# Kernel optimization log

Measured on AMD Instinct MI355X. Metric: run time of the kernel, lower is better.

## Reference

```python
import math
import jax, jax.numpy as jnp
import numpy as np

NEG_INF = -1e9


def maximum_path(neg_cent, text_len, spec_len):
    """Monotonic alignment search (VITS). neg_cent: [B, Ty(spec), Tx(text)].
    Returns hard path [B, Ty, Tx] (float32, 0/1)."""
    B, Ty, Tx = neg_cent.shape
    xs = jnp.arange(Tx)

    # Forward DP over spec frames y; carry = best cumulative value per text pos x.
    def fwd_step(value, inp):
        y, score = inp  # score: [B, Tx]
        diag = jnp.pad(value[:, :-1], ((0, 0), (1, 0)), constant_values=NEG_INF)
        d = diag > value  # move-diagonally indicator for backtracking
        new = score + jnp.maximum(value, diag)
        new = jnp.where(y == 0, jnp.where(xs == 0, score, NEG_INF), new)
        return new, d

    init = jnp.full((B, Tx), NEG_INF, dtype=neg_cent.dtype)
    _, dirs = jax.lax.scan(fwd_step, init,
                           (jnp.arange(Ty), jnp.swapaxes(neg_cent, 0, 1)))
    # dirs: [Ty, B, Tx] bool; dirs[y] compares row y-1 values (as in cython MAS).

    # Backtrack from (spec_len-1, text_len-1) down to y=0.
    def bwd_step(index, inp):
        y, d_row = inp  # index: [B] int32, d_row: [B, Tx]
        active = y < spec_len  # [B]
        row = jnp.where(active[:, None],
                        jax.nn.one_hot(index, Tx, dtype=jnp.float32), 0.0)
        d_at = jnp.take_along_axis(d_row, index[:, None], axis=1)[:, 0]
        move = (index != 0) & ((index == y) | d_at)
        index = jnp.where(active & move, index - 1, index)
        return index, row

    init_idx = text_len - 1
    _, path = jax.lax.scan(bwd_step, init_idx, (jnp.arange(Ty), dirs),
                           reverse=True)
    return jnp.swapaxes(path, 0, 1)  # [B, Ty, Tx]


def setup_inputs() -> dict:
    key = jax.random.key(0)
    ks = jax.random.split(key, 6)
    B, C, Tx, Ty = 8, 192, 512, 2048
    z_p = jax.random.normal(ks[0], (B, C, Ty), dtype=jnp.float32)
    m_p = jax.random.normal(ks[1], (B, C, Tx), dtype=jnp.float32)
    logs_p = 0.1 * jax.random.normal(ks[2], (B, C, Tx), dtype=jnp.float32)
    logs_q = 0.1 * jax.random.normal(ks[3], (B, C, Ty), dtype=jnp.float32)
    text_len = jax.random.randint(ks[4], (B,), Tx * 3 // 4, Tx + 1)
    spec_len = jax.random.randint(ks[5], (B,), Ty * 3 // 4, Ty + 1)
    text_mask = (jnp.arange(Tx)[None, :] < text_len[:, None]).astype(jnp.float32)[:, None, :]
    spec_mask = (jnp.arange(Ty)[None, :] < spec_len[:, None]).astype(jnp.float32)[:, None, :]
    return {"z_p": z_p, "m_p": m_p, "logs_p": logs_p, "logs_q": logs_q,
            "text_mask": text_mask, "spec_mask": spec_mask}


def reference(z_p, m_p, logs_p, logs_q, text_mask, spec_mask):
    text_len = jnp.sum(text_mask, axis=(1, 2)).astype(jnp.int32)  # [B]
    spec_len = jnp.sum(spec_mask, axis=(1, 2)).astype(jnp.int32)  # [B]

    # ---- search_path: neg log-likelihood grid [B, T_spec, T_text] ----
    s_p_sq_r = jnp.exp(-2.0 * logs_p)  # [B, C, Tx]
    nc1 = jnp.sum(-0.5 * math.log(2 * math.pi) - logs_p, axis=1, keepdims=True)  # [B,1,Tx]
    nc2 = jnp.einsum('bct,bcx->btx', -0.5 * z_p * z_p, s_p_sq_r)
    nc3 = jnp.einsum('bct,bcx->btx', z_p, m_p * s_p_sq_r)
    nc4 = jnp.sum(-0.5 * m_p * m_p * s_p_sq_r, axis=1, keepdims=True)  # [B,1,Tx]
    neg_cent = nc1 + nc2 + nc3 + nc4  # [B, Ty, Tx]

    MAS_path = maximum_path(neg_cent, text_len, spec_len)  # [B, Ty, Tx]

    # ---- gather-combine text stats onto spec frames ----
    m_p_a = jnp.einsum('btx,bcx->bct', MAS_path, m_p)      # [B, C, Ty]
    logs_p_a = jnp.einsum('btx,bcx->bct', MAS_path, logs_p)

    # ---- KL divergence loss (VITS) ----
    kl = logs_p_a - logs_q - 0.5 \
        + 0.5 * jnp.square(z_p - m_p_a) * jnp.exp(-2.0 * logs_p_a)
    loss_kl = jnp.sum(kl * spec_mask) / jnp.sum(spec_mask)

    duration = jnp.sum(MAS_path, axis=1)[:, None, :]  # [B, 1, Tx]
    return MAS_path[:, None], m_p_a, logs_p_a, loss_kl, duration
```

## Files before the change

kernel.cpp:

```cpp
#include <hip/hip_runtime.h>
#include <cstdint>
#include <cstddef>

#define BB 8
#define CC 192
#define TXX 512
#define TYY 2048
#define NG_MAX (TYY / 8)

#define NEG_INF (-1e9f)
#define HALF_LOG_2PI 0.9189385332046727f

#define O1 8388608
#define O2 11534336
#define O3 14680064
#define O4 14680065

#define WS_NEG   0
#define WS_S     33554432
#define WS_MSR   36700160
#define WS_BIAS  39845888
#define WS_DIRS  39862272
#define WS_IDX   40910848
#define WS_LENS  40976384
#define WS_PART  40976448

__global__ void k_zero(float* __restrict__ out) {
    int64_t i = (int64_t)blockIdx.x * blockDim.x + threadIdx.x;
    const int64_t n4 = (int64_t)BB * TYY * TXX / 4;
    float4 z4 = make_float4(0.f, 0.f, 0.f, 0.f);
    float4* p4 = (float4*)out;
    for (int64_t k = i; k < n4; k += (int64_t)gridDim.x * blockDim.x) p4[k] = z4;
    if (i < BB * TXX) out[O4 + i] = 0.0f;
}

__global__ void k_prep(const float* __restrict__ logs_p, const float* __restrict__ m_p,
                       float* __restrict__ s, float* __restrict__ msr) {
    int i = blockIdx.x * blockDim.x + threadIdx.x;
    float lp = logs_p[i], m = m_p[i];
    float sv = expf(-2.0f * lp);
    s[i] = sv;
    msr[i] = m * sv;
}

__global__ void k_bias(const float* __restrict__ logs_p, const float* __restrict__ m_p,
                       const float* __restrict__ msr, float* __restrict__ bias) {
    int i = blockIdx.x * blockDim.x + threadIdx.x;
    int b = i >> 9, x = i & (TXX - 1);
    size_t base = (size_t)b * CC * TXX + x;
    const float* lpb = logs_p + base;
    const float* mb  = m_p + base;
    const float* msb = msr + base;
    float acc = 0.f;
#pragma unroll 8
    for (int c = 0; c < CC; ++c)
        acc += -HALF_LOG_2PI - lpb[(size_t)c * TXX] - 0.5f * mb[(size_t)c * TXX] * msb[(size_t)c * TXX];
    bias[i] = acc;
}

__global__ void k_len(const float* __restrict__ tmask, const float* __restrict__ smask,
                      int* __restrict__ lens) {
    __shared__ float red[256];
    int b = blockIdx.x, tid = threadIdx.x;
    float ts = 0.f;
    for (int i = tid; i < TXX; i += 256) ts += tmask[b * TXX + i];
    red[tid] = ts; __syncthreads();
    for (int s = 128; s > 0; s >>= 1) { if (tid < s) red[tid] += red[tid + s]; __syncthreads(); }
    if (tid == 0) lens[b] = (int)(red[0] + 0.5f);
    __syncthreads();
    float ss = 0.f;
    for (int i = tid; i < TYY; i += 256) ss += smask[b * TYY + i];
    red[tid] = ss; __syncthreads();
    for (int s = 128; s > 0; s >>= 1) { if (tid < s) red[tid] += red[tid + s]; __syncthreads(); }
    if (tid == 0) lens[8 + b] = (int)(red[0] + 0.5f);
}

__global__ __launch_bounds__(256) void k_gemm(const float* __restrict__ z,
                                              const float* __restrict__ msr,
                                              const float* __restrict__ sarr,
                                              const float* __restrict__ bias,
                                              const int* __restrict__ lens,
                                              float* __restrict__ neg) {
    int x0 = blockIdx.x * 64, t0 = blockIdx.y * 64, b = blockIdx.z;
    if (x0 >= lens[b] || t0 >= lens[8 + b]) return;

    __shared__ float Zs[16][68], Ms[16][68], Ss[16][68];
    int tid = threadIdx.x;
    int tx = tid & 15, ty = tid >> 4;
    const float* zb = z    + (size_t)b * CC * TYY;
    const float* mb = msr  + (size_t)b * CC * TXX;
    const float* sb = sarr + (size_t)b * CC * TXX;
    int lr = tid >> 4, lc = (tid & 15) * 4;
    float acc[4][4] = {};
    for (int k0 = 0; k0 < CC; k0 += 16) {
        float4 zv = *(const float4*)(zb + (size_t)(k0 + lr) * TYY + t0 + lc);
        float4 mv = *(const float4*)(mb + (size_t)(k0 + lr) * TXX + x0 + lc);
        float4 sv = *(const float4*)(sb + (size_t)(k0 + lr) * TXX + x0 + lc);
        __syncthreads();
        *(float4*)&Zs[lr][lc] = zv;
        *(float4*)&Ms[lr][lc] = mv;
        *(float4*)&Ss[lr][lc] = sv;
        __syncthreads();
#pragma unroll
        for (int k = 0; k < 16; ++k) {
            float4 a4  = *(const float4*)&Zs[k][ty * 4];
            float4 bm4 = *(const float4*)&Ms[k][tx * 4];
            float4 bs4 = *(const float4*)&Ss[k][tx * 4];
            float av[4]  = {a4.x, a4.y, a4.z, a4.w};
            float bmv[4] = {bm4.x, bm4.y, bm4.z, bm4.w};
            float bsv[4] = {bs4.x, bs4.y, bs4.z, bs4.w};
#pragma unroll
            for (int i2 = 0; i2 < 4; ++i2) {
                float a2 = -0.5f * av[i2] * av[i2];
#pragma unroll
                for (int j = 0; j < 4; ++j)
                    acc[i2][j] += av[i2] * bmv[j] + a2 * bsv[j];
            }
        }
    }
    float4 b4 = *(const float4*)(bias + b * TXX + x0 + tx * 4);
    float bv[4] = {b4.x, b4.y, b4.z, b4.w};
#pragma unroll
    for (int i2 = 0; i2 < 4; ++i2) {
        int t = t0 + ty * 4 + i2;
        float4 o;
        o.x = acc[i2][0] + bv[0]; o.y = acc[i2][1] + bv[1];
        o.z = acc[i2][2] + bv[2]; o.w = acc[i2][3] + bv[3];
        *(float4*)(neg + ((size_t)b * TYY + t) * TXX + x0 + tx * 4) = o;
    }
}

#define LOADG(DST, G) do {                                        \
    const float4* gp_ = nc4 + (size_t)(G) * 1024 + 2 * lane;      \
    _Pragma("unroll")                                             \
    for (int r_ = 0; r_ < 8; ++r_) {                              \
        DST[2 * r_]     = gp_[r_ * 128];                          \
        DST[2 * r_ + 1] = gp_[r_ * 128 + 1];                      \
    }                                                             \
} while (0)

#define DPROW(CUR, YB, R) do {                                                \
    int y_ = (YB) + (R);                                                      \
    float s0_ = CUR[2*(R)].x,   s1_ = CUR[2*(R)].y;                           \
    float s2_ = CUR[2*(R)].z,   s3_ = CUR[2*(R)].w;                           \
    float s4_ = CUR[2*(R)+1].x, s5_ = CUR[2*(R)+1].y;                         \
    float s6_ = CUR[2*(R)+1].z, s7_ = CUR[2*(R)+1].w;                         \
    unsigned d_ = 0;                                                          \
    if (y_ == 0) {                                                            \
        if (lane == 0) v[0] = s0_;             \
    } else {                                                                  \
        float pl_ = __int_as_float(__builtin_amdgcn_update_dpp(               \
            0, __float_as_int(v[7]), 0x138, 0xF, 0xF, false));                \
        if (lane == 0) pl_ = NEG_INF;                                         \
        float n0_ = s0_ + fmaxf(v[0], pl_);  if (pl_  > v[0]) d_ |= 1u;       \
        float n1_ = s1_ + fmaxf(v[1], v[0]); if (v[0] > v[1]) d_ |= 2u;       \
        float n2_ = s2_ + fmaxf(v[2], v[1]); if (v[1] > v[2]) d_ |= 4u;       \
        float n3_ = s3_ + fmaxf(v[3], v[2]); if (v[2] > v[3]) d_ |= 8u;       \
        float n4_ = s4_ + fmaxf(v[4], v[3]); if (v[3] > v[4]) d_ |= 16u;      \
        float n5_ = s5_ + fmaxf(v[5], v[4]); if (v[4] > v[5]) d_ |= 32u;      \
        float n6_ = s6_ + fmaxf(v[6], v[5]); if (v[5] > v[6]) d_ |= 64u;      \
        float n7_ = s7_ + fmaxf(v[7], v[6]); if (v[6] > v[7]) d_ |= 128u;     \
        v[0] = n0_; v[1] = n1_; v[2] = n2_; v[3] = n3_;                       \
        v[4] = n4_; v[5] = n5_; v[6] = n6_; v[7] = n7_;                       \
    }                                                                         \
    unsigned t_ = (unsigned)(y_ - 8 * lane);                                  \
    if (t_ < 8u) d_ |= 1u << t_;                 \
    acc |= d_ << (((R) & 3) * 8);                                             \
    if (((R) & 3) == 3) { db32[(y_ >> 2) * 64 + lane] = acc; acc = 0; }       \
} while (0)

#define FWD_ITER(G, CUR, NXT) do {                                \
    int g_ = (G);                                                 \
    if (g_ + 2 < ng) LOADG(NXT, g_ + 2);    \
    int yb_ = 8 * g_;                                             \
    DPROW(CUR, yb_, 0); DPROW(CUR, yb_, 1);                       \
    DPROW(CUR, yb_, 2); DPROW(CUR, yb_, 3);                       \
    DPROW(CUR, yb_, 4); DPROW(CUR, yb_, 5);                       \
    DPROW(CUR, yb_, 6); DPROW(CUR, yb_, 7);                       \
} while (0)

__global__ __launch_bounds__(64, 1) void k_fwd(const float* __restrict__ neg,
                                               const int* __restrict__ lens,
                                               uint32_t* __restrict__ dirs) {
    int b = blockIdx.x, lane = threadIdx.x;
    const float4* nc4 = (const float4*)(neg + (size_t)b * TYY * TXX);
    uint32_t* db32 = dirs + (size_t)b * (TYY / 4) * 64;
    int slen = lens[8 + b];
    int ng = (slen + 7) >> 3;

    float v[8];
#pragma unroll
    for (int j = 0; j < 8; ++j) v[j] = NEG_INF;
    unsigned acc = 0;

    float4 bufA[16], bufB[16], bufC[16];
    LOADG(bufA, 0);
    LOADG(bufB, 1);

    for (int p = 0; p < ng; p += 3) {
        FWD_ITER(p, bufA, bufC);
        if (p + 1 < ng) FWD_ITER(p + 1, bufB, bufA);
        if (p + 2 < ng) FWD_ITER(p + 2, bufC, bufB);
    }
}

__global__ __launch_bounds__(64, 1) void k_bwd(const int* __restrict__ lens,
                                               const uint32_t* __restrict__ dirs,
                                               int* __restrict__ idx_map) {
    int b = blockIdx.x, lane = threadIdx.x;
    const uint32_t* db32 = dirs + (size_t)b * (TYY / 4) * 64;
    int tlen = lens[b], slen = lens[8 + b];

    int idx = tlen - 1;
    int y0 = slen - 1;
    while (y0 >= 0) {
        int nsteps = (y0 + 1 < 32) ? y0 + 1 : 32;
        int y = y0 - lane;
        int yy = (y < 0) ? 0 : y;
        int w0 = (idx >> 5) - 1;
        if (w0 < 0) w0 = 0;
        if (w0 > 14) w0 = 14;
        int qrow = (yy >> 2) * 64;
        int byteoff = (yy & 3) * 8;
        uint32_t lo = 0, hi = 0;
        if (lane < 32) {
#pragma unroll
            for (int k = 0; k < 4; ++k)
                lo |= ((db32[qrow + 4 * w0 + k] >> byteoff) & 0xffu) << (8 * k);
#pragma unroll
            for (int k = 0; k < 4; ++k)
                hi |= ((db32[qrow + 4 * w0 + 4 + k] >> byteoff) & 0xffu) << (8 * k);
        }
        int base = w0 << 5;
        int cap = 0;
#pragma unroll
        for (int j = 0; j < 32; ++j) {
            if (lane == j) cap = idx;
            uint32_t l = (uint32_t)__builtin_amdgcn_readlane((int)lo, j);
            uint32_t h = (uint32_t)__builtin_amdgcn_readlane((int)hi, j);
            int bp = idx - base;
            uint32_t word = (bp & 32) ? h : l;
            int bit = (int)((word >> (bp & 31)) & 1u);
            int move = (int)(idx != 0) & bit;
            idx -= move;
        }
        if (lane < nsteps) idx_map[b * TYY + (y0 - lane)] = cap;
        y0 -= 32;
    }
}

__global__ void k_scatter(const int* __restrict__ lens, const int* __restrict__ idx_map,
                          float* __restrict__ out) {
    int i = blockIdx.x * blockDim.x + threadIdx.x;
    int b = i >> 11, y = i & (TYY - 1);
    if (y < lens[8 + b]) {
        int x = idx_map[i];
        out[(size_t)i * TXX + x] = 1.0f;
        atomicAdd(&out[O4 + b * TXX + x], 1.0f);
    }
}

__global__ __launch_bounds__(256) void k_gather(const float* __restrict__ z_p,
                                                const float* __restrict__ m_p,
                                                const float* __restrict__ logs_p,
                                                const float* __restrict__ logs_q,
                                                const int* __restrict__ lens,
                                                const int* __restrict__ idx_map,
                                                float* __restrict__ out,
                                                float* __restrict__ partials) {
    const int S = BB * CC * TYY / 4;
    int base = blockIdx.x * 256 + threadIdx.x;
    float klsum = 0.f;
#pragma unroll
    for (int r = 0; r < 4; ++r) {
        int i = base + r * S;
        int t = i & (TYY - 1);
        int bc = i >> 11;
        int b = bc / CC;
        float ma = 0.f, la = 0.f;
        if (t < lens[8 + b]) {
            int x = idx_map[b * TYY + t];
            size_t off = (size_t)bc * TXX + x;
            ma = m_p[off];
            la = logs_p[off];
            float zv = z_p[i], lq = logs_q[i];
            float dz = zv - ma;
            klsum += la - lq - 0.5f + 0.5f * dz * dz * expf(-2.0f * la);
        }
        out[O1 + i] = ma;
        out[O2 + i] = la;
    }
    for (int o = 32; o > 0; o >>= 1) klsum += __shfl_down(klsum, o);
    __shared__ float red[4];
    if ((threadIdx.x & 63) == 0) red[threadIdx.x >> 6] = klsum;
    __syncthreads();
    if (threadIdx.x == 0) partials[blockIdx.x] = red[0] + red[1] + red[2] + red[3];
}

__global__ void k_final(const float* __restrict__ partials, const int* __restrict__ lens,
                        float* __restrict__ out) {
    float s = 0.f;
    for (int i = threadIdx.x; i < 3072; i += 256) s += partials[i];
    for (int o = 32; o > 0; o >>= 1) s += __shfl_down(s, o);
    __shared__ float red[4];
    if ((threadIdx.x & 63) == 0) red[threadIdx.x >> 6] = s;
    __syncthreads();
    if (threadIdx.x == 0) {
        float tot = 0.f;
        for (int b = 0; b < 8; ++b) tot += (float)lens[8 + b];
        out[O3] = (red[0] + red[1] + red[2] + red[3]) / tot;
    }
}

extern "C" void kernel_launch(void* const* d_in, const int* in_sizes, int n_in,
                              void* d_out, int out_size, void* d_ws, size_t ws_size,
                              hipStream_t stream) {
    const float* z_p    = (const float*)d_in[0];
    const float* m_p    = (const float*)d_in[1];
    const float* logs_p = (const float*)d_in[2];
    const float* logs_q = (const float*)d_in[3];
    const float* tmask  = (const float*)d_in[4];
    const float* smask  = (const float*)d_in[5];
    float* out = (float*)d_out;
    char* ws = (char*)d_ws;

    float*    neg      = (float*)(ws + WS_NEG);
    float*    sarr     = (float*)(ws + WS_S);
    float*    msr      = (float*)(ws + WS_MSR);
    float*    bias     = (float*)(ws + WS_BIAS);
    uint32_t* dirs     = (uint32_t*)(ws + WS_DIRS);
    int*      idx_map  = (int*)(ws + WS_IDX);
    int*      lens     = (int*)(ws + WS_LENS);
    float*    partials = (float*)(ws + WS_PART);

    hipLaunchKernelGGL(k_zero,    dim3(2048),      dim3(256), 0, stream, out);
    hipLaunchKernelGGL(k_prep,    dim3(3072),      dim3(256), 0, stream, logs_p, m_p, sarr, msr);
    hipLaunchKernelGGL(k_bias,    dim3(16),        dim3(256), 0, stream, logs_p, m_p, msr, bias);
    hipLaunchKernelGGL(k_len,     dim3(8),         dim3(256), 0, stream, tmask, smask, lens);
    hipLaunchKernelGGL(k_gemm,    dim3(8, 32, 8),  dim3(256), 0, stream, z_p, msr, sarr, bias, lens, neg);
    hipLaunchKernelGGL(k_fwd,     dim3(8),         dim3(64),  0, stream, neg, lens, dirs);
    hipLaunchKernelGGL(k_bwd,     dim3(8),         dim3(64),  0, stream, lens, dirs, idx_map);
    hipLaunchKernelGGL(k_scatter, dim3(64),        dim3(256), 0, stream, lens, idx_map, out);
    hipLaunchKernelGGL(k_gather,  dim3(3072),      dim3(256), 0, stream, z_p, m_p, logs_p, logs_q,
                       lens, idx_map, out, partials);
    hipLaunchKernelGGL(k_final,   dim3(1),         dim3(256), 0, stream, partials, lens, out);
}
```

Measured before the change: 593.8 us.

## Stream forward-DP score rows through an LDS ring via async global-to-LDS loads

The single-wave forward DP kernel used to prefetch 8-row groups into three register buffers. It now issues direct global-to-LDS loads into a 4-slot shared-memory ring, staying three groups ahead, and waits on vmcnt before each group. Each lane's two float4 reads use an XOR swizzle on both the global and LDS addresses to avoid bank conflicts. The diagonal-fold bit is also simplified to a per-group compare. This frees registers and deepens the prefetch, at the cost of LDS read latency on the serial DP critical path and of relying on hand-counted vmcnt waits.

Result: slower. 631.2 us (+6.3%).

```diff
diff --git a/kernel.cpp b/kernel.cpp
--- a/kernel.cpp
+++ b/kernel.cpp
@@ -24,6 +24,8 @@
 #define WS_IDX   40910848
 #define WS_LENS  40976384
 #define WS_PART  40976448
+
+typedef float f32x4 __attribute__((ext_vector_type(4)));
 
 __global__ void k_zero(float* __restrict__ out) {
     int64_t i = (int64_t)blockIdx.x * blockDim.x + threadIdx.x;
@@ -130,21 +132,31 @@
     }
 }
 
-#define LOADG(DST, G) do {                                        \
-    const float4* gp_ = nc4 + (size_t)(G) * 1024 + 2 * lane;      \
-    _Pragma("unroll")                                             \
-    for (int r_ = 0; r_ < 8; ++r_) {                              \
-        DST[2 * r_]     = gp_[r_ * 128];                          \
-        DST[2 * r_ + 1] = gp_[r_ * 128 + 1];                      \
-    }                                                             \
+#define WAIT_VM(N) do {                                                   \
+    asm volatile("s_waitcnt vmcnt(" #N ")" ::: "memory");                 \
+    __builtin_amdgcn_sched_barrier(0);                                    \
 } while (0)
 
-#define DPROW(CUR, YB, R) do {                                                \
+#define GLDS(GP, LP)                                                      \
+    __builtin_amdgcn_global_load_lds(                                     \
+        (__attribute__((address_space(1))) void*)(GP),                    \
+        (__attribute__((address_space(3))) void*)(LP), 16, 0, 0)
+
+#define STAGE(G) do {                                                     \
+    const char* gb_ = gsrc + (size_t)(G) * 16384;                         \
+    char* lb_ = ring + (((G) & 3) * 16384);                               \
+    _Pragma("unroll")                                                     \
+    for (int c_ = 0; c_ < 16; ++c_)                                       \
+        GLDS(gb_ + c_ * 1024, lb_ + c_ * 1024);                           \
+} while (0)
+
+#define DPROW(SL, YB, R) do {                                                 \
     int y_ = (YB) + (R);                                                      \
-    float s0_ = CUR[2*(R)].x,   s1_ = CUR[2*(R)].y;                           \
-    float s2_ = CUR[2*(R)].z,   s3_ = CUR[2*(R)].w;                           \
-    float s4_ = CUR[2*(R)+1].x, s5_ = CUR[2*(R)+1].y;                         \
-    float s6_ = CUR[2*(R)+1].z, s7_ = CUR[2*(R)+1].w;                         \
+    const char* rp_ = (SL) + (R) * 2048 + lbase;                              \
+    f32x4 lo_ = *(const f32x4*)(rp_ + sw0);                                   \
+    f32x4 hi_ = *(const f32x4*)(rp_ + sw1);                                   \
+    float s0_ = lo_[0], s1_ = lo_[1], s2_ = lo_[2], s3_ = lo_[3];             \
+    float s4_ = hi_[0], s5_ = hi_[1], s6_ = hi_[2], s7_ = hi_[3];             \
     unsigned d_ = 0;                                                          \
     if (y_ == 0) {                                                            \
         if (lane == 0) v[0] = s0_;             \
@@ -163,27 +175,21 @@
         v[0] = n0_; v[1] = n1_; v[2] = n2_; v[3] = n3_;                       \
         v[4] = n4_; v[5] = n5_; v[6] = n6_; v[7] = n7_;                       \
     }                                                                         \
-    unsigned t_ = (unsigned)(y_ - 8 * lane);                                  \
-    if (t_ < 8u) d_ |= 1u << t_;                 \
+    d_ |= fold_ << (R);                              \
     acc |= d_ << (((R) & 3) * 8);                                             \
     if (((R) & 3) == 3) { db32[(y_ >> 2) * 64 + lane] = acc; acc = 0; }       \
 } while (0)
 
-#define FWD_ITER(G, CUR, NXT) do {                                \
-    int g_ = (G);                                                 \
-    if (g_ + 2 < ng) LOADG(NXT, g_ + 2);    \
-    int yb_ = 8 * g_;                                             \
-    DPROW(CUR, yb_, 0); DPROW(CUR, yb_, 1);                       \
-    DPROW(CUR, yb_, 2); DPROW(CUR, yb_, 3);                       \
-    DPROW(CUR, yb_, 4); DPROW(CUR, yb_, 5);                       \
-    DPROW(CUR, yb_, 6); DPROW(CUR, yb_, 7);                       \
-} while (0)
-
 __global__ __launch_bounds__(64, 1) void k_fwd(const float* __restrict__ neg,
                                                const int* __restrict__ lens,
                                                uint32_t* __restrict__ dirs) {
+    __shared__ __align__(16) char ring[4 * 16384];
     int b = blockIdx.x, lane = threadIdx.x;
-    const float4* nc4 = (const float4*)(neg + (size_t)b * TYY * TXX);
+    unsigned gsw = ((unsigned)lane * 16u) ^ ((((unsigned)lane >> 3) & 1u) << 4);
+    const char* gsrc = (const char*)(neg + (size_t)b * TYY * TXX) + gsw;
+    unsigned lbase = (unsigned)lane * 32u;
+    unsigned sw0 = (((unsigned)lane >> 2) & 1u) << 4;
+    unsigned sw1 = sw0 ^ 16u;
     uint32_t* db32 = dirs + (size_t)b * (TYY / 4) * 64;
     int slen = lens[8 + b];
     int ng = (slen + 7) >> 3;
@@ -193,14 +199,18 @@
     for (int j = 0; j < 8; ++j) v[j] = NEG_INF;
     unsigned acc = 0;
 
-    float4 bufA[16], bufB[16], bufC[16];
-    LOADG(bufA, 0);
-    LOADG(bufB, 1);
-
-    for (int p = 0; p < ng; p += 3) {
-        FWD_ITER(p, bufA, bufC);
-        if (p + 1 < ng) FWD_ITER(p + 1, bufB, bufA);
-        if (p + 2 < ng) FWD_ITER(p + 2, bufC, bufB);
+    STAGE(0); STAGE(1); STAGE(2);
+
+    for (int g = 0; g < ng; ++g) {
+        if (g + 3 < ng)      { STAGE(g + 3); WAIT_VM(48); }
+        else if (g + 2 < ng) { WAIT_VM(32); }
+        else if (g + 1 < ng) { WAIT_VM(16); }
+        else                 { WAIT_VM(0);  }
+        const char* sl = ring + ((g & 3) * 16384);
+        unsigned fold_ = (lane == g) ? 1u : 0u;
+        int yb = 8 * g;
+        DPROW(sl, yb, 0); DPROW(sl, yb, 1); DPROW(sl, yb, 2); DPROW(sl, yb, 3);
+        DPROW(sl, yb, 4); DPROW(sl, yb, 5); DPROW(sl, yb, 6); DPROW(sl, yb, 7);
     }
 }
 
```
